# Performance work log

Measured on AMD Instinct MI355X. Metric: run time of the kernel, lower is better.

## Reference

```python
import jax, jax.numpy as jnp
import numpy as np

N = 8192
D_IN, D_H, D_OUT = 512, 256, 128
BETA = 0.8
EPS = 1e-08


def _xavier(key, fan_in, fan_out):
    limit = float(np.sqrt(6.0 / (fan_in + fan_out)))
    return jax.random.uniform(key, (fan_in, fan_out), jnp.float32, -limit, limit)


def setup_inputs() -> dict:
    key = jax.random.key(0)
    kA, kS, kx, kw1, kw2 = jax.random.split(key, 5)
    A = jax.random.uniform(kA, (N, N), jnp.float32)
    S = jax.random.uniform(kS, (N, N), jnp.float32)
    x = jax.random.normal(kx, (N, D_IN), jnp.float32)
    W1 = _xavier(kw1, D_IN, D_H)
    b1 = jnp.zeros((D_H,), jnp.float32)
    W2 = _xavier(kw2, D_H, D_OUT)
    b2 = jnp.zeros((D_OUT,), jnp.float32)
    return {"A": A, "S": S, "x": x, "W1": W1, "b1": b1, "W2": W2, "b2": b2}


def _normalize_adj(adj):
    # adj + eps * I  (add only on the diagonal; no dense eye materialized)
    idx = jnp.arange(adj.shape[0])
    adj = adj.at[idx, idx].add(EPS)
    d = adj.sum(axis=1)                       # [N]
    d_inv_sqrt = d ** -0.5
    d_inv_sqrt = jnp.where(jnp.isinf(d_inv_sqrt), 0.0, d_inv_sqrt)
    # D^{-1/2} A D^{-1/2} as broadcast row/col scaling (same math as diag matmuls)
    return d_inv_sqrt[:, None] * adj * d_inv_sqrt[None, :]


def reference(A, S, x, W1, b1, W2, b2):
    A_tilde = A + BETA * S                    # [N, N]
    A_norm = _normalize_adj(A_tilde)          # [N, N]
    # GCN layer 1: relu(A_norm @ (x @ W1) + b1)   (dropout is identity at eval)
    h = jax.nn.relu(A_norm @ (x @ W1) + b1)   # [N, D_H]
    # GCN layer 2 (output layer, no activation)
    out = A_norm @ (h @ W2) + b2              # [N, D_OUT]
    return out
```

## Files before the change

### kernel.cpp

```cpp
#include <hip/hip_runtime.h>

#define EPS 1e-8f
#define BETA 0.8f

typedef __attribute__((ext_vector_type(8))) short bf16x8;
typedef __attribute__((ext_vector_type(4))) float f32x4;
typedef __attribute__((ext_vector_type(4))) float float4v;
typedef __attribute__((ext_vector_type(4))) unsigned short ushort4v;

__device__ __forceinline__ unsigned short f2b(float f) {
  unsigned int u = __builtin_bit_cast(unsigned int, f);
  u += 0x7fffu + ((u >> 16) & 1u);
  return (unsigned short)(u >> 16);
}

__global__ __launch_bounds__(256) void k_degree_conv(
    const float* __restrict__ A, const float* __restrict__ S,
    unsigned short* __restrict__ At, float* __restrict__ dis,
    const float* __restrict__ x, unsigned short* __restrict__ xb,
    const float* __restrict__ W1, unsigned short* __restrict__ W1T,
    const float* __restrict__ W2, unsigned short* __restrict__ W2T) {
  __shared__ float wsum[4];
  const int tid = threadIdx.x;
  if (blockIdx.x < 8192) {
    const int row = blockIdx.x;
    const size_t base = (size_t)row * 8192;
    float4v a[8], s[8];
#pragma unroll
    for (int i = 0; i < 8; ++i) {
      const int c = i * 1024 + tid * 4;
      a[i] = __builtin_nontemporal_load(
          reinterpret_cast<const float4v*>(A + base + c));
      s[i] = __builtin_nontemporal_load(
          reinterpret_cast<const float4v*>(S + base + c));
    }
    float sum = 0.f;
#pragma unroll
    for (int i = 0; i < 8; ++i) {
      const int c = i * 1024 + tid * 4;
      float v0 = a[i].x + BETA * s[i].x;
      float v1 = a[i].y + BETA * s[i].y;
      float v2 = a[i].z + BETA * s[i].z;
      float v3 = a[i].w + BETA * s[i].w;
      sum += (v0 + v1) + (v2 + v3);
      ushort4v o = {f2b(v0), f2b(v1), f2b(v2), f2b(v3)};
      *reinterpret_cast<ushort4v*>(At + base + c) = o;
    }
#pragma unroll
    for (int off = 32; off > 0; off >>= 1) sum += __shfl_xor(sum, off, 64);
    if ((tid & 63) == 0) wsum[tid >> 6] = sum;
    __syncthreads();
    if (tid == 0) {
      float d = ((wsum[0] + wsum[1]) + (wsum[2] + wsum[3])) + EPS;
      dis[row] = (d > 0.f) ? 1.0f / sqrtf(d) : 0.f;
    }
  } else {
    const int b = blockIdx.x - 8192;
    if (b < 4096) {
      const int idx = b * 256 + tid;
      float4v v = reinterpret_cast<const float4v*>(x)[idx];
      ushort4v o = {f2b(v.x), f2b(v.y), f2b(v.z), f2b(v.w)};
      reinterpret_cast<ushort4v*>(xb)[idx] = o;
    } else if (b < 4608) {
      const int idx = (b - 4096) * 256 + tid;
      const int r = idx >> 8, c = idx & 255;
      W1T[c * 512 + r] = f2b(W1[idx]);
    } else {
      const int idx = (b - 4608) * 256 + tid;
      const int r = idx >> 7, c = idx & 127;
      W2T[c * 256 + r] = f2b(W2[idx]);
    }
  }
}

__global__ __launch_bounds__(256) void k_conv_all(
    const float* __restrict__ x, unsigned short* __restrict__ xb,
    const float* __restrict__ W1, unsigned short* __restrict__ W1T,
    const float* __restrict__ W2, unsigned short* __restrict__ W2T) {
  const int b = blockIdx.x;
  if (b < 4096) {
    const int idx = b * 256 + threadIdx.x;
    float4v v = reinterpret_cast<const float4v*>(x)[idx];
    ushort4v o = {f2b(v.x), f2b(v.y), f2b(v.z), f2b(v.w)};
    reinterpret_cast<ushort4v*>(xb)[idx] = o;
  } else if (b < 4608) {
    const int idx = (b - 4096) * 256 + threadIdx.x;
    const int r = idx >> 8, c = idx & 255;
    W1T[c * 512 + r] = f2b(W1[idx]);
  } else {
    const int idx = (b - 4608) * 256 + threadIdx.x;
    const int r = idx >> 7, c = idx & 127;
    W2T[c * 256 + r] = f2b(W2[idx]);
  }
}

__global__ __launch_bounds__(256) void k_degree_convert(
    const float* __restrict__ A, const float* __restrict__ S,
    unsigned short* __restrict__ At, float* __restrict__ dis) {
  const int row = blockIdx.x;
  const int tid = threadIdx.x;
  const size_t base = (size_t)row * 8192;
  float4v a[8], s[8];
#pragma unroll
  for (int i = 0; i < 8; ++i) {
    const int c = i * 1024 + tid * 4;
    a[i] = __builtin_nontemporal_load(
        reinterpret_cast<const float4v*>(A + base + c));
    s[i] = __builtin_nontemporal_load(
        reinterpret_cast<const float4v*>(S + base + c));
  }
  float sum = 0.f;
#pragma unroll
  for (int i = 0; i < 8; ++i) {
    const int c = i * 1024 + tid * 4;
    float v0 = a[i].x + BETA * s[i].x;
    float v1 = a[i].y + BETA * s[i].y;
    float v2 = a[i].z + BETA * s[i].z;
    float v3 = a[i].w + BETA * s[i].w;
    sum += (v0 + v1) + (v2 + v3);
    ushort4v o = {f2b(v0), f2b(v1), f2b(v2), f2b(v3)};
    *reinterpret_cast<ushort4v*>(At + base + c) = o;
  }
#pragma unroll
  for (int off = 32; off > 0; off >>= 1) sum += __shfl_xor(sum, off, 64);
  __shared__ float wsum[4];
  if ((tid & 63) == 0) wsum[tid >> 6] = sum;
  __syncthreads();
  if (tid == 0) {
    float d = ((wsum[0] + wsum[1]) + (wsum[2] + wsum[3])) + EPS;
    dis[row] = (d > 0.f) ? 1.0f / sqrtf(d) : 0.f;
  }
}

template <int BM, int BN, int EPI>
__global__ __launch_bounds__(256) void k_gemm_bt(
    const unsigned short* __restrict__ Ag, const unsigned short* __restrict__ BTg,
    int M, int N, int Kstride, int Kchunk,
    const float* __restrict__ dis, const float* __restrict__ bias,
    float* __restrict__ outf, unsigned short* __restrict__ outb) {
  constexpr int WM = BM / 2, WN = BN / 2;
  constexpr int MF = WM / 16, NF = WN / 16;
  constexpr int NLOADS = BM / 32 + BN / 32;
  __shared__ unsigned short Als[2][BM][64];
  __shared__ unsigned short Bls[2][BN][64];
  const int tid = threadIdx.x;
  const int lane = tid & 63;
  const int wm = (tid >> 6) >> 1, wn = (tid >> 6) & 1;
  const int brow = blockIdx.x * BM, bcol = blockIdx.y * BN;
  const int ar = tid >> 3;
  const int ac = (tid & 7) * 8;
  const int l15 = lane & 15, lk = (lane >> 4) * 8;

  f32x4 acc[MF][NF];
#pragma unroll
  for (int i = 0; i < MF; ++i)
#pragma unroll
    for (int j = 0; j < NF; ++j) acc[i][j] = (f32x4){0.f, 0.f, 0.f, 0.f};

  auto stage = [&](int buf, int k0) {
#pragma unroll
    for (int i = 0; i < BM / 32; ++i) {
      const unsigned short* g =
          Ag + (size_t)(brow + i * 32 + ar) * Kstride + k0 + ac;
      __builtin_amdgcn_global_load_lds(
          (const __attribute__((address_space(1))) void*)g,
          (__attribute__((address_space(3))) void*)&Als[buf][i * 32 + ar][ac],
          16, 0, 0);
    }
#pragma unroll
    for (int i = 0; i < BN / 32; ++i) {
      const unsigned short* g =
          BTg + (size_t)(bcol + i * 32 + ar) * Kstride + k0 + ac;
      __builtin_amdgcn_global_load_lds(
          (const __attribute__((address_space(1))) void*)g,
          (__attribute__((address_space(3))) void*)&Bls[buf][i * 32 + ar][ac],
          16, 0, 0);
    }
  };

  const int nsteps = Kchunk / 64;
  stage(0, 0);
  for (int t = 0; t < nsteps; ++t) {
    const int cur = t & 1;
    if (t + 1 < nsteps) {
      stage(cur ^ 1, (t + 1) * 64);
      asm volatile("s_waitcnt vmcnt(%0)" ::"n"(NLOADS));
    } else {
      asm volatile("s_waitcnt vmcnt(0)");
    }
    __builtin_amdgcn_s_barrier();
    asm volatile("" ::: "memory");
#pragma unroll
    for (int kk = 0; kk < 2; ++kk) {
      bf16x8 afr[MF], bfr[NF];
#pragma unroll
      for (int mi = 0; mi < MF; ++mi)
        afr[mi] = *reinterpret_cast<const bf16x8*>(
            &Als[cur][wm * WM + mi * 16 + l15][kk * 32 + lk]);
#pragma unroll
      for (int ni = 0; ni < NF; ++ni)
        bfr[ni] = *reinterpret_cast<const bf16x8*>(
            &Bls[cur][wn * WN + ni * 16 + l15][kk * 32 + lk]);
#pragma unroll
      for (int mi = 0; mi < MF; ++mi)
#pragma unroll
        for (int ni = 0; ni < NF; ++ni)
          acc[mi][ni] = __builtin_amdgcn_mfma_f32_16x16x32_bf16(
              afr[mi], bfr[ni], acc[mi][ni], 0, 0, 0);
    }
    asm volatile("" ::: "memory");
    __builtin_amdgcn_s_barrier();
  }

  const int crow0 = brow + wm * WM, ccol0 = bcol + wn * WN;
#pragma unroll
  for (int mi = 0; mi < MF; ++mi) {
    const int row0 = crow0 + mi * 16 + (lane >> 4) * 4;
    const float d0 = dis[row0], d1 = dis[row0 + 1], d2 = dis[row0 + 2],
                d3 = dis[row0 + 3];
#pragma unroll
    for (int ni = 0; ni < NF; ++ni) {
      const int col = ccol0 + ni * 16 + l15;
      f32x4 a = acc[mi][ni];
      if constexpr (EPI == 0) {
        ushort4v o = {f2b(d0 * a.x), f2b(d1 * a.y), f2b(d2 * a.z),
                      f2b(d3 * a.w)};
        *reinterpret_cast<ushort4v*>(outb + (size_t)col * M + row0) = o;
      } else if constexpr (EPI == 1) {
        const float bb = bias[col];
        float v0 = d0 * a.x + bb; v0 = v0 > 0.f ? v0 : 0.f;
        float v1 = d1 * a.y + bb; v1 = v1 > 0.f ? v1 : 0.f;
        float v2 = d2 * a.z + bb; v2 = v2 > 0.f ? v2 : 0.f;
        float v3 = d3 * a.w + bb; v3 = v3 > 0.f ? v3 : 0.f;
        outb[(size_t)(row0 + 0) * N + col] = f2b(v0);
        outb[(size_t)(row0 + 1) * N + col] = f2b(v1);
        outb[(size_t)(row0 + 2) * N + col] = f2b(v2);
        outb[(size_t)(row0 + 3) * N + col] = f2b(v3);
      } else {
        const float bb = bias[col];
        outf[(size_t)(row0 + 0) * N + col] = d0 * a.x + bb;
        outf[(size_t)(row0 + 1) * N + col] = d1 * a.y + bb;
        outf[(size_t)(row0 + 2) * N + col] = d2 * a.z + bb;
        outf[(size_t)(row0 + 3) * N + col] = d3 * a.w + bb;
      }
    }
  }
}

template <int BM, int BN, int WGM, int WGN>
__global__ __launch_bounds__(512, 2) void k_gemm_split(
    const unsigned short* __restrict__ Ag,
    const unsigned short* __restrict__ BTg,
    int M, int N, int Kstride, int Kchunk, int gx,
    float* __restrict__ P) {
  constexpr int NLOADS = BM / 64 + BN / 64;
  __shared__ unsigned short Als[3][BM][64];
  __shared__ unsigned short Bls[3][BN][64];

  const int nblk = gridDim.x;
  const int flat = blockIdx.x;
  const int cpx = nblk >> 3;
  const int swz = (flat & 7) * cpx + (flat >> 3);
  const int bx = swz % gx;
  const int bz = swz / gx;

  const int tid = threadIdx.x;
  const int lane = tid & 63;
  const int wid = tid >> 6;
  const int wm = wid / WGN, wn = wid % WGN;
  const int brow = bx * BM;
  const int kbase = bz * Kchunk;
  const int ar = tid >> 3;
  const int acs = ((tid & 7) ^ (ar & 7)) * 8;
  const int l15 = lane & 15;
  const int lk = (lane >> 4) * 8;
  const int rk = (l15 & 7) * 8;

  f32x4 acc[4][4];
#pragma unroll
  for (int i = 0; i < 4; ++i)
#pragma unroll
    for (int j = 0; j < 4; ++j) acc[i][j] = (f32x4){0.f, 0.f, 0.f, 0.f};

  auto stage = [&](int buf, int k0) {
#pragma unroll
    for (int i = 0; i < BM / 64; ++i) {
      const unsigned short* g =
          Ag + (size_t)(brow + i * 64 + ar) * Kstride + k0 + acs;
      __builtin_amdgcn_global_load_lds(
          (const __attribute__((address_space(1))) void*)g,
          (__attribute__((address_space(3))) void*)
              &Als[buf][i * 64 + ar][(tid & 7) * 8],
          16, 0, 0);
    }
#pragma unroll
    for (int i = 0; i < BN / 64; ++i) {
      const unsigned short* g =
          BTg + (size_t)(i * 64 + ar) * Kstride + k0 + acs;
      __builtin_amdgcn_global_load_lds(
          (const __attribute__((address_space(1))) void*)g,
          (__attribute__((address_space(3))) void*)
              &Bls[buf][i * 64 + ar][(tid & 7) * 8],
          16, 0, 0);
    }
  };

  const int nsteps = Kchunk / 64;
  stage(0, kbase);
  stage(1, kbase + 64);
  for (int t = 0; t < nsteps; ++t) {
    const int cur = t % 3;
    if (t + 2 < nsteps) {
      stage((t + 2) % 3, kbase + (t + 2) * 64);
      asm volatile("s_waitcnt vmcnt(%0)" ::"n"(2 * NLOADS));
    } else if (t + 1 < nsteps) {
      asm volatile("s_waitcnt vmcnt(%0)" ::"n"(NLOADS));
    } else {
      asm volatile("s_waitcnt vmcnt(0)");
    }
    __builtin_amdgcn_s_barrier();
    asm volatile("" ::: "memory");
#pragma unroll
    for (int kk = 0; kk < 2; ++kk) {
      bf16x8 afr[4], bfr[4];
#pragma unroll
      for (int mi = 0; mi < 4; ++mi)
        afr[mi] = *reinterpret_cast<const bf16x8*>(
            &Als[cur][wm * 64 + mi * 16 + l15][(kk * 32 + lk) ^ rk]);
#pragma unroll
      for (int ni = 0; ni < 4; ++ni)
        bfr[ni] = *reinterpret_cast<const bf16x8*>(
            &Bls[cur][wn * 64 + ni * 16 + l15][(kk * 32 + lk) ^ rk]);
      __builtin_amdgcn_s_setprio(1);
#pragma unroll
      for (int mi = 0; mi < 4; ++mi)
#pragma unroll
        for (int ni = 0; ni < 4; ++ni)
          acc[mi][ni] = __builtin_amdgcn_mfma_f32_16x16x32_bf16(
              afr[mi], bfr[ni], acc[mi][ni], 0, 0, 0);
      __builtin_amdgcn_s_setprio(0);
    }
    asm volatile("" ::: "memory");
    __builtin_amdgcn_s_barrier();
  }

  float* Pz = P + (size_t)bz * M * N;
  const int crow0 = brow + wm * 64, ccol0 = wn * 64;
#pragma unroll
  for (int mi = 0; mi < 4; ++mi) {
    const int row0 = crow0 + mi * 16 + (lane >> 4) * 4;
#pragma unroll
    for (int ni = 0; ni < 4; ++ni) {
      const int col = ccol0 + ni * 16 + l15;
      f32x4 a = acc[mi][ni];
      Pz[(size_t)(row0 + 0) * N + col] = a.x;
      Pz[(size_t)(row0 + 1) * N + col] = a.y;
      Pz[(size_t)(row0 + 2) * N + col] = a.z;
      Pz[(size_t)(row0 + 3) * N + col] = a.w;
    }
  }
}

__global__ __launch_bounds__(512, 4) void k_gemm_l2(
    const unsigned short* __restrict__ Ag,
    const unsigned short* __restrict__ BTg,
    int Kchunk, int gx, float* __restrict__ P) {
  constexpr int M = 8192, N = 128, Kstride = 8192;
  constexpr int NLOADS = 4;
  __shared__ unsigned short Als[2][128][64];
  __shared__ unsigned short Bls[2][128][64];

  const int nblk = gridDim.x;
  const int flat = blockIdx.x;
  const int cpx = nblk >> 3;
  const int swz = (flat & 7) * cpx + (flat >> 3);
  const int bx = swz % gx;
  const int bz = swz / gx;

  const int tid = threadIdx.x;
  const int lane = tid & 63;
  const int wid = tid >> 6;
  const int wm = wid >> 2, wn = wid & 3;
  const int brow = bx * 128;
  const int kbase = bz * Kchunk;
  const int ar = tid >> 3;
  const int acs = ((tid & 7) ^ (ar & 7)) * 8;
  const int l15 = lane & 15;
  const int lk = (lane >> 4) * 8;
  const int rk = (l15 & 7) * 8;

  f32x4 acc[4][2];
#pragma unroll
  for (int i = 0; i < 4; ++i)
#pragma unroll
    for (int j = 0; j < 2; ++j) acc[i][j] = (f32x4){0.f, 0.f, 0.f, 0.f};

  auto stage = [&](int buf, int k0) {
#pragma unroll
    for (int i = 0; i < 2; ++i) {
      const unsigned short* g =
          Ag + (size_t)(brow + i * 64 + ar) * Kstride + k0 + acs;
      __builtin_amdgcn_global_load_lds(
          (const __attribute__((address_space(1))) void*)g,
          (__attribute__((address_space(3))) void*)
              &Als[buf][i * 64 + ar][(tid & 7) * 8],
          16, 0, 0);
    }
#pragma unroll
    for (int i = 0; i < 2; ++i) {
      const unsigned short* g =
          BTg + (size_t)(i * 64 + ar) * Kstride + k0 + acs;
      __builtin_amdgcn_global_load_lds(
          (const __attribute__((address_space(1))) void*)g,
          (__attribute__((address_space(3))) void*)
              &Bls[buf][i * 64 + ar][(tid & 7) * 8],
          16, 0, 0);
    }
  };

  const int nsteps = Kchunk / 64;
  stage(0, kbase);
  for (int t = 0; t < nsteps; ++t) {
    const int cur = t & 1;
    if (t + 1 < nsteps) {
      stage(cur ^ 1, kbase + (t + 1) * 64);
      asm volatile("s_waitcnt vmcnt(%0)" ::"n"(NLOADS));
    } else {
      asm volatile("s_waitcnt vmcnt(0)");
    }
    __builtin_amdgcn_s_barrier();
    asm volatile("" ::: "memory");
#pragma unroll
    for (int kk = 0; kk < 2; ++kk) {
      bf16x8 afr[4], bfr[2];
#pragma unroll
      for (int mi = 0; mi < 4; ++mi)
        afr[mi] = *reinterpret_cast<const bf16x8*>(
            &Als[cur][wm * 64 + mi * 16 + l15][(kk * 32 + lk) ^ rk]);
#pragma unroll
      for (int ni = 0; ni < 2; ++ni)
        bfr[ni] = *reinterpret_cast<const bf16x8*>(
            &Bls[cur][wn * 32 + ni * 16 + l15][(kk * 32 + lk) ^ rk]);
      __builtin_amdgcn_s_setprio(1);
#pragma unroll
      for (int mi = 0; mi < 4; ++mi)
#pragma unroll
        for (int ni = 0; ni < 2; ++ni)
          acc[mi][ni] = __builtin_amdgcn_mfma_f32_16x16x32_bf16(
              afr[mi], bfr[ni], acc[mi][ni], 0, 0, 0);
      __builtin_amdgcn_s_setprio(0);
    }
    asm volatile("" ::: "memory");
    __builtin_amdgcn_s_barrier();
  }

  float* Pz = P + (size_t)bz * M * N;
  const int crow0 = brow + wm * 64, ccol0 = wn * 32;
#pragma unroll
  for (int mi = 0; mi < 4; ++mi) {
    const int row0 = crow0 + mi * 16 + (lane >> 4) * 4;
#pragma unroll
    for (int ni = 0; ni < 2; ++ni) {
      const int col = ccol0 + ni * 16 + l15;
      f32x4 a = acc[mi][ni];
      Pz[(size_t)(row0 + 0) * N + col] = a.x;
      Pz[(size_t)(row0 + 1) * N + col] = a.y;
      Pz[(size_t)(row0 + 2) * N + col] = a.z;
      Pz[(size_t)(row0 + 3) * N + col] = a.w;
    }
  }
}

__global__ __launch_bounds__(256, 2) void k_h_gemm(
    const float* __restrict__ P,
    const unsigned short* __restrict__ W2T,
    const float* __restrict__ dis, const float* __restrict__ b1,
    unsigned short* __restrict__ M2T) {
  __shared__ unsigned short W2ls[128][256];
  __shared__ unsigned short hls[32][256];
  const int tid = threadIdx.x;
  const int lane = tid & 63;
  const int l15 = lane & 15;
  const int wid = tid >> 6;
  const int m0 = blockIdx.x * 32;

  {
    const int wr = tid >> 5, wc = tid & 31;
#pragma unroll
    for (int i = 0; i < 16; ++i) {
      const int row = i * 8 + wr;
      const unsigned short* g = W2T + row * 256 + ((wc ^ (row & 7)) * 8);
      __builtin_amdgcn_global_load_lds(
          (const __attribute__((address_space(1))) void*)g,
          (__attribute__((address_space(3))) void*)&W2ls[row][wc * 8], 16, 0,
          0);
    }
  }

  {
    const int col4 = (tid & 63) * 4;
    const int rsub = tid >> 6;
    const float4v bv = *reinterpret_cast<const float4v*>(b1 + col4);
    const int ch = (tid & 63) >> 1;
    const int sub = (tid & 1) * 4;
#pragma unroll
    for (int p = 0; p < 8; ++p) {
      const int row = p * 4 + rsub;
      const size_t off = (size_t)(m0 + row) * 256 + col4;
      float4v v0 = *reinterpret_cast<const float4v*>(P + off);
      float4v v1 = *reinterpret_cast<const float4v*>(P + 2097152 + off);
      float4v v2 = *reinterpret_cast<const float4v*>(P + 4194304 + off);
      float4v v3 = *reinterpret_cast<const float4v*>(P + 6291456 + off);
      const float dm = dis[m0 + row];
      float r0 = dm * ((v0.x + v1.x) + (v2.x + v3.x)) + bv.x;
      float r1 = dm * ((v0.y + v1.y) + (v2.y + v3.y)) + bv.y;
      float r2 = dm * ((v0.z + v1.z) + (v2.z + v3.z)) + bv.z;
      float r3 = dm * ((v0.w + v1.w) + (v2.w + v3.w)) + bv.w;
      r0 = r0 > 0.f ? r0 : 0.f;
      r1 = r1 > 0.f ? r1 : 0.f;
      r2 = r2 > 0.f ? r2 : 0.f;
      r3 = r3 > 0.f ? r3 : 0.f;
      ushort4v o = {f2b(r0), f2b(r1), f2b(r2), f2b(r3)};
      *reinterpret_cast<ushort4v*>(
          &hls[row][(ch ^ (row & 7)) * 8 + sub]) = o;
    }
  }
  __syncthreads();

  f32x4 acc[2][2];
#pragma unroll
  for (int i = 0; i < 2; ++i)
#pragma unroll
    for (int j = 0; j < 2; ++j) acc[i][j] = (f32x4){0.f, 0.f, 0.f, 0.f};

#pragma unroll
  for (int kk = 0; kk < 8; ++kk) {
    const int gch = kk * 4 + (lane >> 4);
    bf16x8 a[2], b[2];
#pragma unroll
    for (int mi = 0; mi < 2; ++mi) {
      const int mr = mi * 16 + l15;
      a[mi] =
          *reinterpret_cast<const bf16x8*>(&hls[mr][(gch ^ (mr & 7)) * 8]);
    }
#pragma unroll
    for (int ni = 0; ni < 2; ++ni) {
      const int nr = wid * 32 + ni * 16 + l15;
      b[ni] =
          *reinterpret_cast<const bf16x8*>(&W2ls[nr][(gch ^ (nr & 7)) * 8]);
    }
#pragma unroll
    for (int mi = 0; mi < 2; ++mi)
#pragma unroll
      for (int ni = 0; ni < 2; ++ni)
        acc[mi][ni] = __builtin_amdgcn_mfma_f32_16x16x32_bf16(
            a[mi], b[ni], acc[mi][ni], 0, 0, 0);
  }

#pragma unroll
  for (int mi = 0; mi < 2; ++mi) {
    const int r0 = mi * 16 + (lane >> 4) * 4;
    const float d0 = dis[m0 + r0], d1 = dis[m0 + r0 + 1],
                d2 = dis[m0 + r0 + 2], d3 = dis[m0 + r0 + 3];
#pragma unroll
    for (int ni = 0; ni < 2; ++ni) {
      const int col = wid * 32 + ni * 16 + l15;
      f32x4 a = acc[mi][ni];
      ushort4v o = {f2b(d0 * a.x), f2b(d1 * a.y), f2b(d2 * a.z),
                    f2b(d3 * a.w)};
      *reinterpret_cast<ushort4v*>(&M2T[(size_t)col * 8192 + m0 + r0]) = o;
    }
  }
}

template <int MODE, int NS>
__global__ __launch_bounds__(256) void k_reduceN(
    const float* __restrict__ P, int M, int N,
    const float* __restrict__ dis, const float* __restrict__ bias,
    unsigned short* __restrict__ outb, float* __restrict__ outf) {
  const int idx = blockIdx.x * 256 + threadIdx.x;
  const int row = idx / (N / 4);
  const int c0 = (idx - row * (N / 4)) * 4;
  const size_t off = (size_t)row * N + c0;
  const size_t ps = (size_t)M * N;
  float r0 = 0.f, r1 = 0.f, r2 = 0.f, r3 = 0.f;
#pragma unroll
  for (int z = 0; z < NS; ++z) {
    float4v v = *reinterpret_cast<const float4v*>(P + z * ps + off);
    r0 += v.x; r1 += v.y; r2 += v.z; r3 += v.w;
  }
  const float d = dis[row];
  float4v bb = *reinterpret_cast<const float4v*>(bias + c0);
  r0 = d * r0 + bb.x; r1 = d * r1 + bb.y;
  r2 = d * r2 + bb.z; r3 = d * r3 + bb.w;
  if constexpr (MODE == 0) {
    r0 = r0 > 0.f ? r0 : 0.f;
    r1 = r1 > 0.f ? r1 : 0.f;
    r2 = r2 > 0.f ? r2 : 0.f;
    r3 = r3 > 0.f ? r3 : 0.f;
    ushort4v o = {f2b(r0), f2b(r1), f2b(r2), f2b(r3)};
    *reinterpret_cast<ushort4v*>(outb + off) = o;
  } else {
    float4v o = {r0, r1, r2, r3};
    *reinterpret_cast<float4v*>(outf + off) = o;
  }
}

extern "C" void kernel_launch(void* const* d_in, const int* in_sizes, int n_in,
                              void* d_out, int out_size, void* d_ws,
                              size_t ws_size, hipStream_t stream) {
  const float* A  = (const float*)d_in[0];
  const float* S  = (const float*)d_in[1];
  const float* x  = (const float*)d_in[2];
  const float* W1 = (const float*)d_in[3];
  const float* b1 = (const float*)d_in[4];
  const float* W2 = (const float*)d_in[5];
  const float* b2 = (const float*)d_in[6];
  float* out = (float*)d_out;

  char* ws = (char*)d_ws;
  dim3 blk(256);

  const size_t O_At = 0, O_xb = 134217728, O_M1T = 142606336,
               O_P = 146800640, O_W1T = 180355072, O_W2T = 180617216,
               O_dis = 180682752, NEED = 180715520;

  if (ws_size >= NEED) {
    unsigned short* At  = (unsigned short*)(ws + O_At);
    unsigned short* xb  = (unsigned short*)(ws + O_xb);
    unsigned short* M1T = (unsigned short*)(ws + O_M1T);
    float*          P   = (float*)(ws + O_P);
    unsigned short* M2T = (unsigned short*)(ws + O_xb);
    unsigned short* W1T = (unsigned short*)(ws + O_W1T);
    unsigned short* W2T = (unsigned short*)(ws + O_W2T);
    float*          dis = (float*)(ws + O_dis);

    k_degree_conv<<<12928, blk, 0, stream>>>(A, S, At, dis, x, xb, W1, W1T,
                                             W2, W2T);
    k_gemm_bt<128, 64, 0><<<dim3(64, 4), blk, 0, stream>>>(
        xb, W1T, 8192, 256, 512, 512, dis, nullptr, nullptr, M1T);
    k_gemm_split<128, 256, 2, 4><<<dim3(256), dim3(512), 0, stream>>>(
        At, M1T, 8192, 256, 8192, 2048, 64, P);
    k_h_gemm<<<256, blk, 0, stream>>>(P, W2T, dis, b1, M2T);
    k_gemm_l2<<<dim3(512), dim3(512), 0, stream>>>(At, M2T, 1024, 64, P);
    k_reduceN<1, 8><<<1024, blk, 0, stream>>>(P, 8192, 128, dis, b2, nullptr,
                                              out);
  } else {
    unsigned short* At  = (unsigned short*)(ws);
    unsigned short* xb  = (unsigned short*)(ws + 134217728);
    unsigned short* M1T = (unsigned short*)(ws + 142606336);
    unsigned short* hb  = (unsigned short*)(ws + 146800640);
    unsigned short* M2T = (unsigned short*)(ws + 150994944);
    unsigned short* W1T = (unsigned short*)(ws + 153092096);
    unsigned short* W2T = (unsigned short*)(ws + 153354240);
    float* dis          = (float*)(ws + 153419776);

    k_degree_convert<<<8192, blk, 0, stream>>>(A, S, At, dis);
    k_conv_all<<<4736, blk, 0, stream>>>(x, xb, W1, W1T, W2, W2T);
    k_gemm_bt<128, 64, 0><<<dim3(64, 4), blk, 0, stream>>>(
        xb, W1T, 8192, 256, 512, 512, dis, nullptr, nullptr, M1T);
    k_gemm_bt<128, 64, 1><<<dim3(64, 4), blk, 0, stream>>>(
        At, M1T, 8192, 256, 8192, 8192, dis, b1, nullptr, hb);
    k_gemm_bt<64, 64, 0><<<dim3(128, 2), blk, 0, stream>>>(
        hb, W2T, 8192, 128, 256, 256, dis, nullptr, nullptr, M2T);
    k_gemm_bt<64, 64, 2><<<dim3(128, 2), blk, 0, stream>>>(
        At, M2T, 8192, 128, 8192, 8192, dis, b2, out, nullptr);
  }
}
```

Measured before the change: 207.0 us.

## Use 256x256 tiles with 8-way K split for layer-1 adjacency GEMM

Replaces the templated 128x256 layer-1 split-K GEMM with a fixed 256x256 tile kernel: each wave now computes 128x64, K is split 8 ways (Kchunk 1024) instead of 4, and the pipeline drops from triple to double buffering. The larger M tile halves how often the B operand (M1T) is re-read per row of A, and the h-GEMM reduction now sums 8 partial slices instead of 4. The workspace grows for the larger partial buffer, which adds partial-sum write and read traffic. The layer-2 GEMM is generalized with a column-block index but is launched with the same configuration as before.

```diff
diff --git a/kernel.cpp b/kernel.cpp
--- a/kernel.cpp
+++ b/kernel.cpp
@@ -247,28 +247,24 @@
   }
 }
 
-template <int BM, int BN, int WGM, int WGN>
-__global__ __launch_bounds__(512, 2) void k_gemm_split(
+__global__ __launch_bounds__(512, 2) void k_gemm_256(
     const unsigned short* __restrict__ Ag,
     const unsigned short* __restrict__ BTg,
-    int M, int N, int Kstride, int Kchunk, int gx,
-    float* __restrict__ P) {
-  constexpr int NLOADS = BM / 64 + BN / 64;
-  __shared__ unsigned short Als[3][BM][64];
-  __shared__ unsigned short Bls[3][BN][64];
-
-  const int nblk = gridDim.x;
+    int Kchunk, float* __restrict__ P) {
+  constexpr int Kstride = 8192, N = 256;
+  __shared__ unsigned short Als[2][256][64];
+  __shared__ unsigned short Bls[2][256][64];
+
   const int flat = blockIdx.x;
-  const int cpx = nblk >> 3;
-  const int swz = (flat & 7) * cpx + (flat >> 3);
-  const int bx = swz % gx;
-  const int bz = swz / gx;
+  const int swz = (flat & 7) * 32 + (flat >> 3);
+  const int bx = swz & 31;
+  const int bz = swz >> 5;
 
   const int tid = threadIdx.x;
   const int lane = tid & 63;
   const int wid = tid >> 6;
-  const int wm = wid / WGN, wn = wid % WGN;
-  const int brow = bx * BM;
+  const int wm = wid >> 2, wn = wid & 3;
+  const int brow = bx * 256;
   const int kbase = bz * Kchunk;
   const int ar = tid >> 3;
   const int acs = ((tid & 7) ^ (ar & 7)) * 8;
@@ -276,15 +272,15 @@
   const int lk = (lane >> 4) * 8;
   const int rk = (l15 & 7) * 8;
 
-  f32x4 acc[4][4];
-#pragma unroll
-  for (int i = 0; i < 4; ++i)
+  f32x4 acc[8][4];
+#pragma unroll
+  for (int i = 0; i < 8; ++i)
 #pragma unroll
     for (int j = 0; j < 4; ++j) acc[i][j] = (f32x4){0.f, 0.f, 0.f, 0.f};
 
   auto stage = [&](int buf, int k0) {
 #pragma unroll
-    for (int i = 0; i < BM / 64; ++i) {
+    for (int i = 0; i < 4; ++i) {
       const unsigned short* g =
           Ag + (size_t)(brow + i * 64 + ar) * Kstride + k0 + acs;
       __builtin_amdgcn_global_load_lds(
@@ -294,7 +290,7 @@
           16, 0, 0);
     }
 #pragma unroll
-    for (int i = 0; i < BN / 64; ++i) {
+    for (int i = 0; i < 4; ++i) {
       const unsigned short* g =
           BTg + (size_t)(i * 64 + ar) * Kstride + k0 + acs;
       __builtin_amdgcn_global_load_lds(
@@ -307,14 +303,11 @@
 
   const int nsteps = Kchunk / 64;
   stage(0, kbase);
-  stage(1, kbase + 64);
   for (int t = 0; t < nsteps; ++t) {
-    const int cur = t % 3;
-    if (t + 2 < nsteps) {
-      stage((t + 2) % 3, kbase + (t + 2) * 64);
-      asm volatile("s_waitcnt vmcnt(%0)" ::"n"(2 * NLOADS));
-    } else if (t + 1 < nsteps) {
-      asm volatile("s_waitcnt vmcnt(%0)" ::"n"(NLOADS));
+    const int cur = t & 1;
+    if (t + 1 < nsteps) {
+      stage(cur ^ 1, kbase + (t + 1) * 64);
+      asm volatile("s_waitcnt vmcnt(8)");
     } else {
       asm volatile("s_waitcnt vmcnt(0)");
     }
@@ -322,18 +315,18 @@
     asm volatile("" ::: "memory");
 #pragma unroll
     for (int kk = 0; kk < 2; ++kk) {
-      bf16x8 afr[4], bfr[4];
-#pragma unroll
-      for (int mi = 0; mi < 4; ++mi)
+      bf16x8 afr[8], bfr[4];
+#pragma unroll
+      for (int mi = 0; mi < 8; ++mi)
         afr[mi] = *reinterpret_cast<const bf16x8*>(
-            &Als[cur][wm * 64 + mi * 16 + l15][(kk * 32 + lk) ^ rk]);
+            &Als[cur][wm * 128 + mi * 16 + l15][(kk * 32 + lk) ^ rk]);
 #pragma unroll
       for (int ni = 0; ni < 4; ++ni)
         bfr[ni] = *reinterpret_cast<const bf16x8*>(
             &Bls[cur][wn * 64 + ni * 16 + l15][(kk * 32 + lk) ^ rk]);
       __builtin_amdgcn_s_setprio(1);
 #pragma unroll
-      for (int mi = 0; mi < 4; ++mi)
+      for (int mi = 0; mi < 8; ++mi)
 #pragma unroll
         for (int ni = 0; ni < 4; ++ni)
           acc[mi][ni] = __builtin_amdgcn_mfma_f32_16x16x32_bf16(
@@ -344,10 +337,10 @@
     __builtin_amdgcn_s_barrier();
   }
 
-  float* Pz = P + (size_t)bz * M * N;
-  const int crow0 = brow + wm * 64, ccol0 = wn * 64;
-#pragma unroll
-  for (int mi = 0; mi < 4; ++mi) {
+  float* Pz = P + (size_t)bz * 8192 * N;
+  const int crow0 = brow + wm * 128, ccol0 = wn * 64;
+#pragma unroll
+  for (int mi = 0; mi < 8; ++mi) {
     const int row0 = crow0 + mi * 16 + (lane >> 4) * 4;
 #pragma unroll
     for (int ni = 0; ni < 4; ++ni) {
@@ -361,11 +354,12 @@
   }
 }
 
-__global__ __launch_bounds__(512, 4) void k_gemm_l2(
+__global__ __launch_bounds__(512, 4) void k_gemm_big(
     const unsigned short* __restrict__ Ag,
     const unsigned short* __restrict__ BTg,
-    int Kchunk, int gx, float* __restrict__ P) {
-  constexpr int M = 8192, N = 128, Kstride = 8192;
+    int N, int Kchunk, int gx, int ncol,
+    float* __restrict__ P) {
+  constexpr int M = 8192, Kstride = 8192;
   constexpr int NLOADS = 4;
   __shared__ unsigned short Als[2][128][64];
   __shared__ unsigned short Bls[2][128][64];
@@ -375,13 +369,16 @@
   const int cpx = nblk >> 3;
   const int swz = (flat & 7) * cpx + (flat >> 3);
   const int bx = swz % gx;
-  const int bz = swz / gx;
+  const int rem = swz / gx;
+  const int by = rem % ncol;
+  const int bz = rem / ncol;
 
   const int tid = threadIdx.x;
   const int lane = tid & 63;
   const int wid = tid >> 6;
   const int wm = wid >> 2, wn = wid & 3;
   const int brow = bx * 128;
+  const int bcol = by * 128;
   const int kbase = bz * Kchunk;
   const int ar = tid >> 3;
   const int acs = ((tid & 7) ^ (ar & 7)) * 8;
@@ -409,7 +406,7 @@
 #pragma unroll
     for (int i = 0; i < 2; ++i) {
       const unsigned short* g =
-          BTg + (size_t)(i * 64 + ar) * Kstride + k0 + acs;
+          BTg + (size_t)(bcol + i * 64 + ar) * Kstride + k0 + acs;
       __builtin_amdgcn_global_load_lds(
           (const __attribute__((address_space(1))) void*)g,
           (__attribute__((address_space(3))) void*)
@@ -455,7 +452,7 @@
   }
 
   float* Pz = P + (size_t)bz * M * N;
-  const int crow0 = brow + wm * 64, ccol0 = wn * 32;
+  const int crow0 = brow + wm * 64, ccol0 = bcol + wn * 32;
 #pragma unroll
   for (int mi = 0; mi < 4; ++mi) {
     const int row0 = crow0 + mi * 16 + (lane >> 4) * 4;
@@ -507,15 +504,18 @@
     for (int p = 0; p < 8; ++p) {
       const int row = p * 4 + rsub;
       const size_t off = (size_t)(m0 + row) * 256 + col4;
-      float4v v0 = *reinterpret_cast<const float4v*>(P + off);
-      float4v v1 = *reinterpret_cast<const float4v*>(P + 2097152 + off);
-      float4v v2 = *reinterpret_cast<const float4v*>(P + 4194304 + off);
-      float4v v3 = *reinterpret_cast<const float4v*>(P + 6291456 + off);
+      float r0 = 0.f, r1 = 0.f, r2 = 0.f, r3 = 0.f;
+#pragma unroll
+      for (int z = 0; z < 8; ++z) {
+        float4v v =
+            *reinterpret_cast<const float4v*>(P + (size_t)z * 2097152 + off);
+        r0 += v.x; r1 += v.y; r2 += v.z; r3 += v.w;
+      }
       const float dm = dis[m0 + row];
-      float r0 = dm * ((v0.x + v1.x) + (v2.x + v3.x)) + bv.x;
-      float r1 = dm * ((v0.y + v1.y) + (v2.y + v3.y)) + bv.y;
-      float r2 = dm * ((v0.z + v1.z) + (v2.z + v3.z)) + bv.z;
-      float r3 = dm * ((v0.w + v1.w) + (v2.w + v3.w)) + bv.w;
+      r0 = dm * r0 + bv.x;
+      r1 = dm * r1 + bv.y;
+      r2 = dm * r2 + bv.z;
+      r3 = dm * r3 + bv.w;
       r0 = r0 > 0.f ? r0 : 0.f;
       r1 = r1 > 0.f ? r1 : 0.f;
       r2 = r2 > 0.f ? r2 : 0.f;
@@ -622,8 +622,8 @@
   dim3 blk(256);
 
   const size_t O_At = 0, O_xb = 134217728, O_M1T = 142606336,
-               O_P = 146800640, O_W1T = 180355072, O_W2T = 180617216,
-               O_dis = 180682752, NEED = 180715520;
+               O_P = 146800640, O_W1T = 213909504, O_W2T = 214171648,
+               O_dis = 214237184, NEED = 214269952;
 
   if (ws_size >= NEED) {
     unsigned short* At  = (unsigned short*)(ws + O_At);
@@ -639,10 +639,10 @@
                                              W2, W2T);
     k_gemm_bt<128, 64, 0><<<dim3(64, 4), blk, 0, stream>>>(
         xb, W1T, 8192, 256, 512, 512, dis, nullptr, nullptr, M1T);
-    k_gemm_split<128, 256, 2, 4><<<dim3(256), dim3(512), 0, stream>>>(
-        At, M1T, 8192, 256, 8192, 2048, 64, P);
+    k_gemm_256<<<dim3(256), dim3(512), 0, stream>>>(At, M1T, 1024, P);
     k_h_gemm<<<256, blk, 0, stream>>>(P, W2T, dis, b1, M2T);
-    k_gemm_l2<<<dim3(512), dim3(512), 0, stream>>>(At, M2T, 1024, 64, P);
+    k_gemm_big<<<dim3(512), dim3(512), 0, stream>>>(At, M2T, 128, 1024, 64, 1,
+                                                    P);
     k_reduceN<1, 8><<<1024, blk, 0, stream>>>(P, 8192, 128, dis, b2, nullptr,
                                               out);
   } else {
```

Measured after the change: 207.5 us. Within noise of the previous version (+0.2%).
